# Performance work log

Measured on AMD Instinct MI355X. Metric: run time of the kernel, lower is better.

The kernel has to match this reference:

```python
import jax, jax.numpy as jnp
import numpy as np

N_ATOMS = 100000
M_NBR = 12
ORIG_FEA = 92
NBR_FEA = 41
AF = 64          # atom_fea_len
N_CONV = 3
OUT_DIM = 128
N_CRYSTALS = 2000
ATOMS_PER = 50
EPS = 1e-5


def setup_inputs() -> dict:
    key = jax.random.key(0)
    ks = jax.random.split(key, 12)
    inp = {
        "atom_fea": jax.random.normal(ks[0], (N_ATOMS, ORIG_FEA), dtype=jnp.float32),
        "nbr_fea": jax.random.normal(ks[1], (N_ATOMS, M_NBR, NBR_FEA), dtype=jnp.float32),
        "nbr_fea_idx": jax.random.randint(ks[2], (N_ATOMS, M_NBR), 0, N_ATOMS, dtype=jnp.int32),
        "crystal_atom_idx": jnp.arange(N_CRYSTALS * ATOMS_PER, dtype=jnp.int32).reshape(N_CRYSTALS, ATOMS_PER),
    }
    # parameters
    inp["W_embed"] = jax.random.normal(ks[3], (ORIG_FEA, AF), dtype=jnp.float32) * 0.05
    inp["b_embed"] = jnp.zeros((AF,), dtype=jnp.float32)
    in_full = 2 * AF + NBR_FEA  # 169
    inp["W_full"] = jax.random.normal(ks[4], (N_CONV, in_full, 2 * AF), dtype=jnp.float32) * 0.05
    inp["b_full"] = jnp.zeros((N_CONV, 2 * AF), dtype=jnp.float32)
    inp["bn1_gamma"] = jnp.ones((N_CONV, 2 * AF), dtype=jnp.float32)
    inp["bn1_beta"] = jnp.zeros((N_CONV, 2 * AF), dtype=jnp.float32)
    inp["bn2_gamma"] = jnp.ones((N_CONV, AF), dtype=jnp.float32)
    inp["bn2_beta"] = jnp.zeros((N_CONV, AF), dtype=jnp.float32)
    inp["W_pool"] = jax.random.normal(ks[5], (AF, OUT_DIM), dtype=jnp.float32) * 0.05
    inp["b_pool"] = jnp.zeros((OUT_DIM,), dtype=jnp.float32)
    return inp


def _batchnorm(x, gamma, beta):
    # training-mode BatchNorm1d over leading dim, biased variance
    m = jnp.mean(x, axis=0)
    v = jnp.var(x, axis=0)
    return (x - m) * jax.lax.rsqrt(v + EPS) * gamma + beta


def _conv_layer(x, nbr_fea, nbr_fea_idx, Wf, bf, g1, be1, g2, be2):
    N, M = nbr_fea_idx.shape
    nbr_atom = x[nbr_fea_idx]                                  # [N, M, AF] gather
    self_fea = jnp.broadcast_to(x[:, None, :], (N, M, AF))     # [N, M, AF]
    total = jnp.concatenate([self_fea, nbr_atom, nbr_fea], axis=2)  # [N, M, 2AF+NBR]
    gated = jnp.einsum('nmi,io->nmo', total, Wf) + bf          # [N, M, 2AF]
    gated = _batchnorm(gated.reshape(N * M, 2 * AF), g1, be1).reshape(N, M, 2 * AF)
    nbr_filter = jax.nn.sigmoid(gated[..., :AF])
    nbr_core = jax.nn.softplus(gated[..., AF:])
    nbr_sumed = jnp.sum(nbr_filter * nbr_core, axis=1)         # [N, AF]
    nbr_sumed = _batchnorm(nbr_sumed, g2, be2)
    return jax.nn.softplus(x + nbr_sumed)


def reference(atom_fea, nbr_fea, nbr_fea_idx, crystal_atom_idx,
              W_embed, b_embed, W_full, b_full,
              bn1_gamma, bn1_beta, bn2_gamma, bn2_beta,
              W_pool, b_pool):
    x = atom_fea @ W_embed + b_embed                           # [N, AF]
    for i in range(N_CONV):
        x = _conv_layer(x, nbr_fea, nbr_fea_idx,
                        W_full[i], b_full[i],
                        bn1_gamma[i], bn1_beta[i],
                        bn2_gamma[i], bn2_beta[i])
    crystal_fea = jnp.mean(x[crystal_atom_idx], axis=1)        # [G, AF] per-graph mean pool
    return jax.nn.relu(crystal_fea @ W_pool + b_pool)          # [G, OUT_DIM]
```

## Files before the change

### kernel.cpp

```cpp
#include <hip/hip_runtime.h>
#include <hip/hip_fp16.h>
#include <math.h>

#define N_ATOMS 100000
#define M_NBR 12
#define ORIG_FEA 92
#define NBR_FEA 41
#define AF 64
#define OUT2 128
#define IN_FULL 169
#define N_CONV 3
#define OUT_DIM 128
#define N_CRYSTALS 2000
#define ATOMS_PER 50
#define EPS 1e-5f

#define ZCH 16
#define EDGES (ZCH * M_NBR)
#define NF_STRIDE 44
#define YB_ATOMS 80
#define YB_CHUNK 16
#define ZP_BLOCKS 1024

typedef _Float16 h4 __attribute__((ext_vector_type(4)));

__device__ __forceinline__ float softplus_f(float x) {
    return fmaxf(x, 0.0f) + __logf(1.0f + __expf(-fabsf(x)));
}
__device__ __forceinline__ float sigmoid_f(float x) {
    return __builtin_amdgcn_rcpf(1.0f + __expf(-x));
}
__device__ __forceinline__ void fma4(float4& a, float s, const float4& b) {
    a.x = fmaf(s, b.x, a.x); a.y = fmaf(s, b.y, a.y);
    a.z = fmaf(s, b.z, a.z); a.w = fmaf(s, b.w, a.w);
}
__device__ __forceinline__ float4 zero4() { return make_float4(0.f, 0.f, 0.f, 0.f); }

union H4 { uint2 u; __half2 h[2]; };
__device__ __forceinline__ void store_h4(__half* p, float4 v) {
    H4 t;
    t.h[0] = __floats2half2_rn(v.x, v.y);
    t.h[1] = __floats2half2_rn(v.z, v.w);
    *(uint2*)p = t.u;
}
__device__ __forceinline__ float4 load_h4(const __half* p) {
    H4 t; t.u = *(const uint2*)p;
    float2 a = __half22float2(t.h[0]);
    float2 b = __half22float2(t.h[1]);
    return make_float4(a.x, a.y, b.x, b.y);
}

__global__ __launch_bounds__(256, 2) void k_embed(
    const float* __restrict__ af, const float* __restrict__ W,
    const float* __restrict__ b, float* __restrict__ x) {
  __shared__ __align__(16) float saf[64 * ORIG_FEA];
  int a0 = blockIdx.x * 64;
  int na = min(64, N_ATOMS - a0);
  int tid = threadIdx.x;
  int c = tid & 63, rgrp = tid >> 6;
  float w[ORIG_FEA];
#pragma unroll
  for (int k = 0; k < ORIG_FEA; ++k) w[k] = W[k * AF + c];
  int n4 = na * (ORIG_FEA / 4);
  const float4* g4 = (const float4*)(af + (size_t)a0 * ORIG_FEA);
  float4* s4 = (float4*)saf;
  for (int e = tid; e < n4; e += 256) s4[e] = g4[e];
  __syncthreads();
  float bc = b[c];
  for (int a = rgrp; a < na; a += 4) {
    float acc = bc;
    const float4* row = (const float4*)(saf + a * ORIG_FEA);
#pragma unroll
    for (int q = 0; q < ORIG_FEA / 4; ++q) {
      float4 v = row[q];
      acc = fmaf(v.x, w[4 * q], acc);
      acc = fmaf(v.y, w[4 * q + 1], acc);
      acc = fmaf(v.z, w[4 * q + 2], acc);
      acc = fmaf(v.w, w[4 * q + 3], acc);
    }
    x[(size_t)(a0 + a) * AF + c] = acc;
  }
}

__global__ __launch_bounds__(256, 2) void k_ysn(
    const float* __restrict__ x, const float* __restrict__ Wf,
    float* __restrict__ y_self, float* __restrict__ y_nbr) {
  __shared__ __align__(16) float sW2[64 * 256];
  __shared__ __align__(16) float sx[YB_CHUNK * AF];
  int tid = threadIdx.x;
  int cg = tid & 31, ag = tid >> 5;
  int c0 = cg * 4;
  {
    float4* s4 = (float4*)sW2;
    const float4* g4 = (const float4*)Wf;
    for (int e = tid; e < 64 * 64; e += 256) {
      int r = e >> 6, q = e & 63;
      s4[r * 64 + q] = (q < 32) ? g4[r * 32 + q] : g4[(64 + r) * 32 + (q - 32)];
    }
  }
  int ab = blockIdx.x * YB_ATOMS;
  for (int cc = 0; cc < YB_ATOMS / YB_CHUNK; ++cc) {
    int a0 = ab + cc * YB_CHUNK;
    __syncthreads();
    {
      float4* s4 = (float4*)sx;
      const float4* g4 = (const float4*)(x + (size_t)a0 * AF);
      for (int e = tid; e < YB_CHUNK * AF / 4; e += 256) s4[e] = g4[e];
    }
    __syncthreads();
    float4 accs[2] = {zero4(), zero4()};
    float4 accn[2] = {zero4(), zero4()};
    for (int k0 = 0; k0 < AF; k0 += 4) {
      float4 av0 = *(const float4*)(sx + (ag * 2 + 0) * AF + k0);
      float4 av1 = *(const float4*)(sx + (ag * 2 + 1) * AF + k0);
#pragma unroll
      for (int kk = 0; kk < 4; ++kk) {
        float4 b0 = *(const float4*)(sW2 + (k0 + kk) * 256 + c0);
        float4 b1 = *(const float4*)(sW2 + (k0 + kk) * 256 + 128 + c0);
        float s0 = (kk == 0) ? av0.x : (kk == 1) ? av0.y : (kk == 2) ? av0.z : av0.w;
        float s1 = (kk == 0) ? av1.x : (kk == 1) ? av1.y : (kk == 2) ? av1.z : av1.w;
        fma4(accs[0], s0, b0); fma4(accn[0], s0, b1);
        fma4(accs[1], s1, b0); fma4(accn[1], s1, b1);
      }
    }
#pragma unroll
    for (int t = 0; t < 2; ++t) {
      size_t n = (size_t)(a0 + ag * 2 + t);
      *(float4*)(y_self + n * OUT2 + c0) = accs[t];
      *(float4*)(y_nbr + n * OUT2 + c0) = accn[t];
    }
  }
}

__device__ __forceinline__ void edge_gemm(
    const _Float16* snf, const float* sW, int ebase, int c0,
    float4 acc0[6], float4 acc1[6]) {
#pragma unroll
  for (int e = 0; e < 6; ++e) { acc0[e] = zero4(); acc1[e] = zero4(); }
  for (int k0 = 0; k0 < 40; k0 += 4) {
    h4 av[6];
#pragma unroll
    for (int e = 0; e < 6; ++e)
      av[e] = *(const h4*)(snf + (ebase + e) * NF_STRIDE + k0);
#pragma unroll
    for (int kk = 0; kk < 4; ++kk) {
      float4 b0 = *(const float4*)(sW + (k0 + kk) * OUT2 + c0);
      float4 b1 = *(const float4*)(sW + (k0 + kk) * OUT2 + AF + c0);
#pragma unroll
      for (int e = 0; e < 6; ++e) {
        float s = (float)av[e][kk];
        fma4(acc0[e], s, b0);
        fma4(acc1[e], s, b1);
      }
    }
  }
  {
    float4 b0 = *(const float4*)(sW + 40 * OUT2 + c0);
    float4 b1 = *(const float4*)(sW + 40 * OUT2 + AF + c0);
#pragma unroll
    for (int e = 0; e < 6; ++e) {
      float s = (float)snf[(ebase + e) * NF_STRIDE + 40];
      fma4(acc0[e], s, b0);
      fma4(acc1[e], s, b1);
    }
  }
}

template <int WZ>
__global__ __launch_bounds__(256, 2) void k_zstats_p(
    const float* __restrict__ nbr_fea, const int* __restrict__ nidx,
    const float* __restrict__ y_self, const float* __restrict__ y_nbr,
    const float* __restrict__ Wf, const float* __restrict__ bf,
    float* __restrict__ gsum, float* __restrict__ gsumsq,
    __half* __restrict__ z16) {
  __shared__ __align__(16) _Float16 snf[EDGES * NF_STRIDE];
  __shared__ __align__(16) float sW[NBR_FEA * OUT2];
  __shared__ __align__(16) unsigned char sbuf[1024];
  int* sidx = (int*)sbuf;
  int tid = threadIdx.x;
  int cg = tid & 15, eg = tid >> 4;
  int c0 = cg * 4;
  {
    float4* sW4 = (float4*)sW;
    const float4* gW4 = (const float4*)(Wf + 2 * AF * OUT2);
    for (int e = tid; e < NBR_FEA * (OUT2 / 4); e += 256) sW4[e] = gW4[e];
  }
  float4 bz0 = *(const float4*)(bf + c0);
  float4 bz1 = *(const float4*)(bf + AF + c0);
  float4 sm0 = zero4(), sq0 = zero4(), sm1 = zero4(), sq1 = zero4();
  for (int cc = blockIdx.x; cc < N_ATOMS / ZCH; cc += ZP_BLOCKS) {
    int a0 = cc * ZCH;
    __syncthreads();
    const float* gnf = nbr_fea + (size_t)a0 * M_NBR * NBR_FEA;
    for (int e = tid; e < EDGES * NBR_FEA; e += 256) {
      int r = e / NBR_FEA;
      int k = e - r * NBR_FEA;
      snf[r * NF_STRIDE + k] = (_Float16)gnf[e];
    }
    for (int e = tid; e < EDGES; e += 256) {
      snf[e * NF_STRIDE + 41] = (_Float16)0.f;
      snf[e * NF_STRIDE + 42] = (_Float16)0.f;
      snf[e * NF_STRIDE + 43] = (_Float16)0.f;
      sidx[e] = nidx[(size_t)a0 * M_NBR + e];
    }
    __syncthreads();
    for (int c = 0; c < 2; ++c) {
      int ebase = c * 96 + eg * 6;
      int atomL = c * 8 + (eg >> 1);
      const float* ys = y_self + (size_t)(a0 + atomL) * OUT2;
      float4 y0 = *(const float4*)(ys + c0);
      float4 y1 = *(const float4*)(ys + AF + c0);
      float4 acc0[6], acc1[6];
      edge_gemm(snf, sW, ebase, c0, acc0, acc1);
#pragma unroll
      for (int e = 0; e < 6; ++e) {
        int j = sidx[ebase + e];
        const float* yn = y_nbr + (size_t)j * OUT2;
        float4 n0 = *(const float4*)(yn + c0);
        float4 n1 = *(const float4*)(yn + AF + c0);
        float4 z0, z1;
        z0.x = acc0[e].x + y0.x + n0.x + bz0.x; z0.y = acc0[e].y + y0.y + n0.y + bz0.y;
        z0.z = acc0[e].z + y0.z + n0.z + bz0.z; z0.w = acc0[e].w + y0.w + n0.w + bz0.w;
        z1.x = acc1[e].x + y1.x + n1.x + bz1.x; z1.y = acc1[e].y + y1.y + n1.y + bz1.y;
        z1.z = acc1[e].z + y1.z + n1.z + bz1.z; z1.w = acc1[e].w + y1.w + n1.w + bz1.w;
        if (WZ) {
          __half* zp = z16 + ((size_t)a0 * M_NBR + ebase + e) * OUT2 + c0;
          store_h4(zp, z0);
          store_h4(zp + AF, z1);
        }
        sm0.x += z0.x; sm0.y += z0.y; sm0.z += z0.z; sm0.w += z0.w;
        sm1.x += z1.x; sm1.y += z1.y; sm1.z += z1.z; sm1.w += z1.w;
        sq0.x = fmaf(z0.x, z0.x, sq0.x); sq0.y = fmaf(z0.y, z0.y, sq0.y);
        sq0.z = fmaf(z0.z, z0.z, sq0.z); sq0.w = fmaf(z0.w, z0.w, sq0.w);
        sq1.x = fmaf(z1.x, z1.x, sq1.x); sq1.y = fmaf(z1.y, z1.y, sq1.y);
        sq1.z = fmaf(z1.z, z1.z, sq1.z); sq1.w = fmaf(z1.w, z1.w, sq1.w);
      }
    }
  }
  __syncthreads();
  float* lsum = (float*)sbuf;
  float* lsumsq = lsum + OUT2;
  ((float*)sbuf)[tid] = 0.f;
  __syncthreads();
  atomicAdd(&lsum[c0 + 0], sm0.x); atomicAdd(&lsum[c0 + 1], sm0.y);
  atomicAdd(&lsum[c0 + 2], sm0.z); atomicAdd(&lsum[c0 + 3], sm0.w);
  atomicAdd(&lsum[AF + c0 + 0], sm1.x); atomicAdd(&lsum[AF + c0 + 1], sm1.y);
  atomicAdd(&lsum[AF + c0 + 2], sm1.z); atomicAdd(&lsum[AF + c0 + 3], sm1.w);
  atomicAdd(&lsumsq[c0 + 0], sq0.x); atomicAdd(&lsumsq[c0 + 1], sq0.y);
  atomicAdd(&lsumsq[c0 + 2], sq0.z); atomicAdd(&lsumsq[c0 + 3], sq0.w);
  atomicAdd(&lsumsq[AF + c0 + 0], sq1.x); atomicAdd(&lsumsq[AF + c0 + 1], sq1.y);
  atomicAdd(&lsumsq[AF + c0 + 2], sq1.z); atomicAdd(&lsumsq[AF + c0 + 3], sq1.w);
  __syncthreads();
  if (tid < OUT2) {
    atomicAdd(&gsum[tid], lsum[tid]);
    atomicAdd(&gsumsq[tid], lsumsq[tid]);
  }
}

__device__ __forceinline__ void stage_edge(
    const float* __restrict__ nbr_fea, const int* __restrict__ nidx,
    const float* __restrict__ We, int a0, int tid,
    _Float16* snf, float* sW, int* sidx) {
  float4* sW4 = (float4*)sW;
  const float4* gW4 = (const float4*)We;
  for (int e = tid; e < NBR_FEA * (OUT2 / 4); e += 256) sW4[e] = gW4[e];
  const float* gnf = nbr_fea + (size_t)a0 * M_NBR * NBR_FEA;
  for (int e = tid; e < EDGES * NBR_FEA; e += 256) {
    int r = e / NBR_FEA;
    int k = e - r * NBR_FEA;
    snf[r * NF_STRIDE + k] = (_Float16)gnf[e];
  }
  for (int e = tid; e < EDGES; e += 256) {
    snf[e * NF_STRIDE + 41] = (_Float16)0.f;
    snf[e * NF_STRIDE + 42] = (_Float16)0.f;
    snf[e * NF_STRIDE + 43] = (_Float16)0.f;
    sidx[e] = nidx[(size_t)a0 * M_NBR + e];
  }
}

__global__ __launch_bounds__(256, 2) void k_zstats_fb(
    const float* __restrict__ nbr_fea, const int* __restrict__ nidx,
    const float* __restrict__ y_self, const float* __restrict__ y_nbr,
    const float* __restrict__ Wf, const float* __restrict__ bf,
    float* __restrict__ gsum, float* __restrict__ gsumsq) {
  __shared__ __align__(16) _Float16 snf[EDGES * NF_STRIDE];
  __shared__ __align__(16) float sW[NBR_FEA * OUT2];
  __shared__ int sidx[EDGES];
  __shared__ float lsum[OUT2], lsumsq[OUT2];
  int tid = threadIdx.x;
  int cg = tid & 15, eg = tid >> 4;
  int c0 = cg * 4;
  if (tid < OUT2) { lsum[tid] = 0.f; lsumsq[tid] = 0.f; }
  int a0 = blockIdx.x * ZCH;
  stage_edge(nbr_fea, nidx, Wf + 2 * AF * OUT2, a0, tid, snf, sW, sidx);
  __syncthreads();
  float4 bz0 = *(const float4*)(bf + c0);
  float4 bz1 = *(const float4*)(bf + AF + c0);
  float4 sm0 = zero4(), sq0 = zero4(), sm1 = zero4(), sq1 = zero4();
  for (int c = 0; c < 2; ++c) {
    int ebase = c * 96 + eg * 6;
    int atomL = c * 8 + (eg >> 1);
    const float* ys = y_self + (size_t)(a0 + atomL) * OUT2;
    float4 y0 = *(const float4*)(ys + c0);
    float4 y1 = *(const float4*)(ys + AF + c0);
    float4 acc0[6], acc1[6];
    edge_gemm(snf, sW, ebase, c0, acc0, acc1);
#pragma unroll
    for (int e = 0; e < 6; ++e) {
      int j = sidx[ebase + e];
      const float* yn = y_nbr + (size_t)j * OUT2;
      float4 n0 = *(const float4*)(yn + c0);
      float4 n1 = *(const float4*)(yn + AF + c0);
      float4 z0, z1;
      z0.x = acc0[e].x + y0.x + n0.x + bz0.x; z0.y = acc0[e].y + y0.y + n0.y + bz0.y;
      z0.z = acc0[e].z + y0.z + n0.z + bz0.z; z0.w = acc0[e].w + y0.w + n0.w + bz0.w;
      z1.x = acc1[e].x + y1.x + n1.x + bz1.x; z1.y = acc1[e].y + y1.y + n1.y + bz1.y;
      z1.z = acc1[e].z + y1.z + n1.z + bz1.z; z1.w = acc1[e].w + y1.w + n1.w + bz1.w;
      sm0.x += z0.x; sm0.y += z0.y; sm0.z += z0.z; sm0.w += z0.w;
      sm1.x += z1.x; sm1.y += z1.y; sm1.z += z1.z; sm1.w += z1.w;
      sq0.x = fmaf(z0.x, z0.x, sq0.x); sq0.y = fmaf(z0.y, z0.y, sq0.y);
      sq0.z = fmaf(z0.z, z0.z, sq0.z); sq0.w = fmaf(z0.w, z0.w, sq0.w);
      sq1.x = fmaf(z1.x, z1.x, sq1.x); sq1.y = fmaf(z1.y, z1.y, sq1.y);
      sq1.z = fmaf(z1.z, z1.z, sq1.z); sq1.w = fmaf(z1.w, z1.w, sq1.w);
    }
  }
  atomicAdd(&lsum[c0 + 0], sm0.x); atomicAdd(&lsum[c0 + 1], sm0.y);
  atomicAdd(&lsum[c0 + 2], sm0.z); atomicAdd(&lsum[c0 + 3], sm0.w);
  atomicAdd(&lsum[AF + c0 + 0], sm1.x); atomicAdd(&lsum[AF + c0 + 1], sm1.y);
  atomicAdd(&lsum[AF + c0 + 2], sm1.z); atomicAdd(&lsum[AF + c0 + 3], sm1.w);
  atomicAdd(&lsumsq[c0 + 0], sq0.x); atomicAdd(&lsumsq[c0 + 1], sq0.y);
  atomicAdd(&lsumsq[c0 + 2], sq0.z); atomicAdd(&lsumsq[c0 + 3], sq0.w);
  atomicAdd(&lsumsq[AF + c0 + 0], sq1.x); atomicAdd(&lsumsq[AF + c0 + 1], sq1.y);
  atomicAdd(&lsumsq[AF + c0 + 2], sq1.z); atomicAdd(&lsumsq[AF + c0 + 3], sq1.w);
  __syncthreads();
  if (tid < OUT2) {
    atomicAdd(&gsum[tid], lsum[tid]);
    atomicAdd(&gsumsq[tid], lsumsq[tid]);
  }
}

__global__ __launch_bounds__(256, 4) void k_apply_stream(
    const __half* __restrict__ z16,
    const float* __restrict__ sc1, const float* __restrict__ sh1,
    float* __restrict__ s_out, float* __restrict__ gsum, float* __restrict__ gsumsq) {
  __shared__ float lsum[AF], lsumsq[AF];
  int tid = threadIdx.x;
  if (tid < AF) { lsum[tid] = 0.f; lsumsq[tid] = 0.f; }
  __syncthreads();
  int cg = tid & 15, a = tid >> 4;
  int c0 = cg * 4;
  size_t atom = (size_t)blockIdx.x * 16 + a;
  float4 f0 = *(const float4*)(sc1 + c0);
  float4 g0 = *(const float4*)(sh1 + c0);
  float4 f1 = *(const float4*)(sc1 + AF + c0);
  float4 g1 = *(const float4*)(sh1 + AF + c0);
  const __half* zr = z16 + atom * (M_NBR * OUT2);
  float4 sacc = zero4();
#pragma unroll 4
  for (int m = 0; m < M_NBR; ++m) {
    float4 zf = load_h4(zr + m * OUT2 + c0);
    float4 zc = load_h4(zr + m * OUT2 + AF + c0);
    zf.x = fmaf(zf.x, f0.x, g0.x); zf.y = fmaf(zf.y, f0.y, g0.y);
    zf.z = fmaf(zf.z, f0.z, g0.z); zf.w = fmaf(zf.w, f0.w, g0.w);
    zc.x = fmaf(zc.x, f1.x, g1.x); zc.y = fmaf(zc.y, f1.y, g1.y);
    zc.z = fmaf(zc.z, f1.z, g1.z); zc.w = fmaf(zc.w, f1.w, g1.w);
    sacc.x = fmaf(sigmoid_f(zf.x), softplus_f(zc.x), sacc.x);
    sacc.y = fmaf(sigmoid_f(zf.y), softplus_f(zc.y), sacc.y);
    sacc.z = fmaf(sigmoid_f(zf.z), softplus_f(zc.z), sacc.z);
    sacc.w = fmaf(sigmoid_f(zf.w), softplus_f(zc.w), sacc.w);
  }
  *(float4*)(s_out + atom * AF + c0) = sacc;
  float4 sq;
  sq.x = sacc.x * sacc.x; sq.y = sacc.y * sacc.y;
  sq.z = sacc.z * sacc.z; sq.w = sacc.w * sacc.w;
  sacc.x += __shfl_xor(sacc.x, 16, 64); sacc.y += __shfl_xor(sacc.y, 16, 64);
  sacc.z += __shfl_xor(sacc.z, 16, 64); sacc.w += __shfl_xor(sacc.w, 16, 64);
  sq.x += __shfl_xor(sq.x, 16, 64); sq.y += __shfl_xor(sq.y, 16, 64);
  sq.z += __shfl_xor(sq.z, 16, 64); sq.w += __shfl_xor(sq.w, 16, 64);
  sacc.x += __shfl_xor(sacc.x, 32, 64); sacc.y += __shfl_xor(sacc.y, 32, 64);
  sacc.z += __shfl_xor(sacc.z, 32, 64); sacc.w += __shfl_xor(sacc.w, 32, 64);
  sq.x += __shfl_xor(sq.x, 32, 64); sq.y += __shfl_xor(sq.y, 32, 64);
  sq.z += __shfl_xor(sq.z, 32, 64); sq.w += __shfl_xor(sq.w, 32, 64);
  if ((tid & 48) == 0) {
    atomicAdd(&lsum[c0 + 0], sacc.x); atomicAdd(&lsum[c0 + 1], sacc.y);
    atomicAdd(&lsum[c0 + 2], sacc.z); atomicAdd(&lsum[c0 + 3], sacc.w);
    atomicAdd(&lsumsq[c0 + 0], sq.x); atomicAdd(&lsumsq[c0 + 1], sq.y);
    atomicAdd(&lsumsq[c0 + 2], sq.z); atomicAdd(&lsumsq[c0 + 3], sq.w);
  }
  __syncthreads();
  if (tid < AF) {
    atomicAdd(&gsum[tid], lsum[tid]);
    atomicAdd(&gsumsq[tid], lsumsq[tid]);
  }
}

__global__ __launch_bounds__(256, 2) void k_apply(
    const float* __restrict__ nbr_fea, const int* __restrict__ nidx,
    const float* __restrict__ y_self, const float* __restrict__ y_nbr,
    const float* __restrict__ Wf, const float* __restrict__ bf,
    const float* __restrict__ sc1, const float* __restrict__ sh1,
    float* __restrict__ s_out, float* __restrict__ gsum, float* __restrict__ gsumsq) {
  __shared__ __align__(16) _Float16 snf[EDGES * NF_STRIDE];
  __shared__ __align__(16) float sW[NBR_FEA * OUT2];
  __shared__ int sidx[EDGES];
  __shared__ float lsum[AF], lsumsq[AF];
  int tid = threadIdx.x;
  int cg = tid & 15, eg = tid >> 4;
  int c0 = cg * 4;
  if (tid < AF) { lsum[tid] = 0.f; lsumsq[tid] = 0.f; }
  int a0 = blockIdx.x * ZCH;
  stage_edge(nbr_fea, nidx, Wf + 2 * AF * OUT2, a0, tid, snf, sW, sidx);
  __syncthreads();
  float4 bz0 = *(const float4*)(bf + c0);
  float4 bz1 = *(const float4*)(bf + AF + c0);
  float4 f0 = *(const float4*)(sc1 + c0);
  float4 g0 = *(const float4*)(sh1 + c0);
  float4 f1 = *(const float4*)(sc1 + AF + c0);
  float4 g1 = *(const float4*)(sh1 + AF + c0);
  for (int c = 0; c < 2; ++c) {
    int ebase = c * 96 + eg * 6;
    int atomL = c * 8 + (eg >> 1);
    const float* ys = y_self + (size_t)(a0 + atomL) * OUT2;
    float4 y0 = *(const float4*)(ys + c0);
    float4 y1 = *(const float4*)(ys + AF + c0);
    float4 acc0[6], acc1[6];
    edge_gemm(snf, sW, ebase, c0, acc0, acc1);
    float4 sacc = zero4();
#pragma unroll
    for (int e = 0; e < 6; ++e) {
      int j = sidx[ebase + e];
      const float* yn = y_nbr + (size_t)j * OUT2;
      float4 n0 = *(const float4*)(yn + c0);
      float4 n1 = *(const float4*)(yn + AF + c0);
      float4 z0, z1;
      z0.x = fmaf(acc0[e].x + y0.x + n0.x + bz0.x, f0.x, g0.x);
      z0.y = fmaf(acc0[e].y + y0.y + n0.y + bz0.y, f0.y, g0.y);
      z0.z = fmaf(acc0[e].z + y0.z + n0.z + bz0.z, f0.z, g0.z);
      z0.w = fmaf(acc0[e].w + y0.w + n0.w + bz0.w, f0.w, g0.w);
      z1.x = fmaf(acc1[e].x + y1.x + n1.x + bz1.x, f1.x, g1.x);
      z1.y = fmaf(acc1[e].y + y1.y + n1.y + bz1.y, f1.y, g1.y);
      z1.z = fmaf(acc1[e].z + y1.z + n1.z + bz1.z, f1.z, g1.z);
      z1.w = fmaf(acc1[e].w + y1.w + n1.w + bz1.w, f1.w, g1.w);
      sacc.x = fmaf(sigmoid_f(z0.x), softplus_f(z1.x), sacc.x);
      sacc.y = fmaf(sigmoid_f(z0.y), softplus_f(z1.y), sacc.y);
      sacc.z = fmaf(sigmoid_f(z0.z), softplus_f(z1.z), sacc.z);
      sacc.w = fmaf(sigmoid_f(z0.w), softplus_f(z1.w), sacc.w);
    }
    sacc.x += __shfl_xor(sacc.x, 16, 64);
    sacc.y += __shfl_xor(sacc.y, 16, 64);
    sacc.z += __shfl_xor(sacc.z, 16, 64);
    sacc.w += __shfl_xor(sacc.w, 16, 64);
    if ((eg & 1) == 0) {
      *(float4*)(s_out + (size_t)(a0 + atomL) * AF + c0) = sacc;
      atomicAdd(&lsum[c0 + 0], sacc.x); atomicAdd(&lsum[c0 + 1], sacc.y);
      atomicAdd(&lsum[c0 + 2], sacc.z); atomicAdd(&lsum[c0 + 3], sacc.w);
      atomicAdd(&lsumsq[c0 + 0], sacc.x * sacc.x);
      atomicAdd(&lsumsq[c0 + 1], sacc.y * sacc.y);
      atomicAdd(&lsumsq[c0 + 2], sacc.z * sacc.z);
      atomicAdd(&lsumsq[c0 + 3], sacc.w * sacc.w);
    }
  }
  __syncthreads();
  if (tid < AF) {
    atomicAdd(&gsum[tid], lsum[tid]);
    atomicAdd(&gsumsq[tid], lsumsq[tid]);
  }
}

__global__ void k_finalize(const float* __restrict__ gsum, const float* __restrict__ gsumsq,
                           const float* __restrict__ gamma, const float* __restrict__ beta,
                           float* __restrict__ scale, float* __restrict__ shift,
                           int chn, float invcount) {
  int c = threadIdx.x;
  if (c < chn) {
    float m = gsum[c] * invcount;
    float v = gsumsq[c] * invcount - m * m;
    float sc = gamma[c] * rsqrtf(v + EPS);
    scale[c] = sc;
    shift[c] = beta[c] - m * sc;
  }
}

__global__ __launch_bounds__(256) void k_update(
    float* __restrict__ x, const float* __restrict__ s,
    const float* __restrict__ sc2, const float* __restrict__ sh2) {
  int e = blockIdx.x * 256 + threadIdx.x;
  if (e < N_ATOMS * AF) {
    int c = e & (AF - 1);
    float v = x[e] + s[e] * sc2[c] + sh2[c];
    x[e] = softplus_f(v);
  }
}

__global__ __launch_bounds__(128) void k_pool(
    const float* __restrict__ x, const int* __restrict__ cidx,
    const float* __restrict__ Wp, const float* __restrict__ bp,
    float* __restrict__ out) {
  __shared__ float part[2][AF];
  __shared__ float mean[AF];
  int g = blockIdx.x, tid = threadIdx.x;
  int c = tid & 63, h = tid >> 6;
  float acc = 0.f;
  for (int a = h; a < ATOMS_PER; a += 2) {
    int idx = cidx[g * ATOMS_PER + a];
    acc += x[(size_t)idx * AF + c];
  }
  part[h][c] = acc;
  __syncthreads();
  if (tid < AF) mean[tid] = (part[0][tid] + part[1][tid]) * (1.0f / ATOMS_PER);
  __syncthreads();
  float o = bp[tid];
#pragma unroll
  for (int k = 0; k < AF; ++k) o += mean[k] * Wp[k * OUT_DIM + tid];
  out[(size_t)g * OUT_DIM + tid] = fmaxf(o, 0.f);
}

extern "C" void kernel_launch(void* const* d_in, const int* in_sizes, int n_in,
                              void* d_out, int out_size, void* d_ws, size_t ws_size,
                              hipStream_t stream) {
  const float* atom_fea = (const float*)d_in[0];
  const float* nbr_fea  = (const float*)d_in[1];
  const int*   nbr_idx  = (const int*)d_in[2];
  const int*   cidx     = (const int*)d_in[3];
  const float* W_embed  = (const float*)d_in[4];
  const float* b_embed  = (const float*)d_in[5];
  const float* W_full   = (const float*)d_in[6];
  const float* b_full   = (const float*)d_in[7];
  const float* bn1_g    = (const float*)d_in[8];
  const float* bn1_b    = (const float*)d_in[9];
  const float* bn2_g    = (const float*)d_in[10];
  const float* bn2_b    = (const float*)d_in[11];
  const float* W_pool   = (const float*)d_in[12];
  const float* b_pool   = (const float*)d_in[13];
  float* out = (float*)d_out;

  float* ws = (float*)d_ws;
  size_t off = 0;
  float* x      = ws + off; off += (size_t)N_ATOMS * AF;
  float* y_self = ws + off; off += (size_t)N_ATOMS * OUT2;
  float* y_nbr  = ws + off; off += (size_t)N_ATOMS * OUT2;
  float* s_buf  = ws + off; off += (size_t)N_ATOMS * AF;
  float* sums   = ws + off; off += (size_t)N_CONV * 384;
  float* affine = ws + off; off += (size_t)N_CONV * 384;

  size_t base_bytes = (off * sizeof(float) + 255) & ~(size_t)255;
  size_t z_bytes = (size_t)N_ATOMS * M_NBR * OUT2 * sizeof(__half);
  bool fast = ws_size >= base_bytes + z_bytes;
  __half* z16 = fast ? (__half*)((char*)d_ws + base_bytes) : nullptr;

  hipMemsetAsync(sums, 0, (size_t)N_CONV * 384 * sizeof(float), stream);

  k_embed<<<(N_ATOMS + 63) / 64, 256, 0, stream>>>(atom_fea, W_embed, b_embed, x);

  for (int i = 0; i < N_CONV; ++i) {
    const float* Wf = W_full + (size_t)i * IN_FULL * OUT2;
    const float* bf = b_full + (size_t)i * OUT2;
    float* sum1   = sums + (size_t)i * 384;
    float* sumsq1 = sum1 + OUT2;
    float* sum2   = sumsq1 + OUT2;
    float* sumsq2 = sum2 + AF;
    float* sc1 = affine + (size_t)i * 384;
    float* sh1 = sc1 + OUT2;
    float* sc2 = sh1 + OUT2;
    float* sh2 = sc2 + AF;

    k_ysn<<<N_ATOMS / YB_ATOMS, 256, 0, stream>>>(x, Wf, y_self, y_nbr);
    if (fast) {
      k_zstats_p<1><<<ZP_BLOCKS, 256, 0, stream>>>(
          nbr_fea, nbr_idx, y_self, y_nbr, Wf, bf, sum1, sumsq1, z16);
    } else {
      k_zstats_fb<<<N_ATOMS / ZCH, 256, 0, stream>>>(
          nbr_fea, nbr_idx, y_self, y_nbr, Wf, bf, sum1, sumsq1);
    }
    k_finalize<<<1, 128, 0, stream>>>(sum1, sumsq1, bn1_g + i * OUT2, bn1_b + i * OUT2,
                                      sc1, sh1, OUT2, 1.0f / ((float)N_ATOMS * M_NBR));
    if (fast) {
      k_apply_stream<<<N_ATOMS / 16, 256, 0, stream>>>(z16, sc1, sh1, s_buf,
                                                       sum2, sumsq2);
    } else {
      k_apply<<<N_ATOMS / ZCH, 256, 0, stream>>>(nbr_fea, nbr_idx, y_self, y_nbr,
                                                 Wf, bf, sc1, sh1, s_buf, sum2, sumsq2);
    }
    k_finalize<<<1, 128, 0, stream>>>(sum2, sumsq2, bn2_g + i * AF, bn2_b + i * AF,
                                      sc2, sh2, AF, 1.0f / (float)N_ATOMS);
    k_update<<<(N_ATOMS * AF + 255) / 256, 256, 0, stream>>>(x, s_buf, sc2, sh2);
  }

  k_pool<<<N_CRYSTALS, 128, 0, stream>>>(x, cidx, W_pool, b_pool, out);
}
```

Before: 1.967 ms.

## Double-buffer neighbor feature staging in zstats kernel

The zstats kernel now stages the next chunk's neighbor features and indices into a second shared-memory buffer while computing on the current chunk, which removes one barrier per iteration. The aim is to overlap global loads with the edge GEMM and the neighbor gathers. In exchange, shared memory per block roughly doubles for the feature tile, which may cut occupancy below the two blocks per CU the launch bounds ask for. The loads are synchronous stores into LDS, so the actual overlap depends on how the compiler schedules them.

```diff
diff --git a/kernel.cpp b/kernel.cpp
--- a/kernel.cpp
+++ b/kernel.cpp
@@ -21,6 +21,7 @@
 #define YB_ATOMS 80
 #define YB_CHUNK 16
 #define ZP_BLOCKS 1024
+#define NCHUNKS (N_ATOMS / ZCH)
 
 typedef _Float16 h4 __attribute__((ext_vector_type(4)));
 
@@ -173,10 +174,9 @@
     const float* __restrict__ Wf, const float* __restrict__ bf,
     float* __restrict__ gsum, float* __restrict__ gsumsq,
     __half* __restrict__ z16) {
-  __shared__ __align__(16) _Float16 snf[EDGES * NF_STRIDE];
+  __shared__ __align__(16) _Float16 snf[2 * EDGES * NF_STRIDE];
   __shared__ __align__(16) float sW[NBR_FEA * OUT2];
-  __shared__ __align__(16) unsigned char sbuf[1024];
-  int* sidx = (int*)sbuf;
+  __shared__ __align__(16) unsigned char sbuf[1536];
   int tid = threadIdx.x;
   int cg = tid & 15, eg = tid >> 4;
   int c0 = cg * 4;
@@ -185,25 +185,50 @@
     const float4* gW4 = (const float4*)(Wf + 2 * AF * OUT2);
     for (int e = tid; e < NBR_FEA * (OUT2 / 4); e += 256) sW4[e] = gW4[e];
   }
+  {
+    int a0 = blockIdx.x * ZCH;
+    const float* gnf = nbr_fea + (size_t)a0 * M_NBR * NBR_FEA;
+    _Float16* s = snf;
+    int* si = (int*)sbuf;
+    for (int e = tid; e < EDGES * NBR_FEA; e += 256) {
+      int r = e / NBR_FEA;
+      int k = e - r * NBR_FEA;
+      s[r * NF_STRIDE + k] = (_Float16)gnf[e];
+    }
+    for (int e = tid; e < EDGES; e += 256) {
+      s[e * NF_STRIDE + 41] = (_Float16)0.f;
+      s[e * NF_STRIDE + 42] = (_Float16)0.f;
+      s[e * NF_STRIDE + 43] = (_Float16)0.f;
+      si[e] = nidx[(size_t)a0 * M_NBR + e];
+    }
+  }
+  __syncthreads();
   float4 bz0 = *(const float4*)(bf + c0);
   float4 bz1 = *(const float4*)(bf + AF + c0);
   float4 sm0 = zero4(), sq0 = zero4(), sm1 = zero4(), sq1 = zero4();
-  for (int cc = blockIdx.x; cc < N_ATOMS / ZCH; cc += ZP_BLOCKS) {
+  int buf = 0;
+  for (int cc = blockIdx.x; cc < NCHUNKS; cc += ZP_BLOCKS) {
+    int ccn = cc + ZP_BLOCKS;
+    if (ccn < NCHUNKS) {
+      int an = ccn * ZCH;
+      const float* gnf = nbr_fea + (size_t)an * M_NBR * NBR_FEA;
+      _Float16* s = snf + (buf ^ 1) * (EDGES * NF_STRIDE);
+      int* si = (int*)sbuf + (buf ^ 1) * EDGES;
+      for (int e = tid; e < EDGES * NBR_FEA; e += 256) {
+        int r = e / NBR_FEA;
+        int k = e - r * NBR_FEA;
+        s[r * NF_STRIDE + k] = (_Float16)gnf[e];
+      }
+      for (int e = tid; e < EDGES; e += 256) {
+        s[e * NF_STRIDE + 41] = (_Float16)0.f;
+        s[e * NF_STRIDE + 42] = (_Float16)0.f;
+        s[e * NF_STRIDE + 43] = (_Float16)0.f;
+        si[e] = nidx[(size_t)an * M_NBR + e];
+      }
+    }
     int a0 = cc * ZCH;
-    __syncthreads();
-    const float* gnf = nbr_fea + (size_t)a0 * M_NBR * NBR_FEA;
-    for (int e = tid; e < EDGES * NBR_FEA; e += 256) {
-      int r = e / NBR_FEA;
-      int k = e - r * NBR_FEA;
-      snf[r * NF_STRIDE + k] = (_Float16)gnf[e];
-    }
-    for (int e = tid; e < EDGES; e += 256) {
-      snf[e * NF_STRIDE + 41] = (_Float16)0.f;
-      snf[e * NF_STRIDE + 42] = (_Float16)0.f;
-      snf[e * NF_STRIDE + 43] = (_Float16)0.f;
-      sidx[e] = nidx[(size_t)a0 * M_NBR + e];
-    }
-    __syncthreads();
+    const _Float16* scur = snf + buf * (EDGES * NF_STRIDE);
+    const int* sicur = (const int*)sbuf + buf * EDGES;
     for (int c = 0; c < 2; ++c) {
       int ebase = c * 96 + eg * 6;
       int atomL = c * 8 + (eg >> 1);
@@ -211,10 +236,10 @@
       float4 y0 = *(const float4*)(ys + c0);
       float4 y1 = *(const float4*)(ys + AF + c0);
       float4 acc0[6], acc1[6];
-      edge_gemm(snf, sW, ebase, c0, acc0, acc1);
+      edge_gemm(scur, sW, ebase, c0, acc0, acc1);
 #pragma unroll
       for (int e = 0; e < 6; ++e) {
-        int j = sidx[ebase + e];
+        int j = sicur[ebase + e];
         const float* yn = y_nbr + (size_t)j * OUT2;
         float4 n0 = *(const float4*)(yn + c0);
         float4 n1 = *(const float4*)(yn + AF + c0);
@@ -236,8 +261,9 @@
         sq1.z = fmaf(z1.z, z1.z, sq1.z); sq1.w = fmaf(z1.w, z1.w, sq1.w);
       }
     }
-  }
-  __syncthreads();
+    __syncthreads();
+    buf ^= 1;
+  }
   float* lsum = (float*)sbuf;
   float* lsumsq = lsum + OUT2;
   ((float*)sbuf)[tid] = 0.f;
```

Result: faster. 1.872 ms (-4.9%).
